# Performance work log

Hardware: AMD Instinct MI355X
Metric: run time of the kernel (lower is better)

## Reference

```python
import jax, jax.numpy as jnp
import numpy as np

WAVE_LEN = 1000.0
DIM_G = 64


def box_relational_embedding(boxes):
    # boxes: (B, N, 4) -> (B, N, N, 64) trigonometric geometry embedding
    B, N, _ = boxes.shape
    x_min, y_min, x_max, y_max = jnp.split(boxes, 4, axis=-1)  # each (B,N,1)
    cx = (x_min + x_max) * 0.5
    cy = (y_min + y_max) * 0.5
    w = (x_max - x_min) + 1.0
    h = (y_max - y_min) + 1.0
    cxT = jnp.swapaxes(cx, 1, 2)  # (B,1,N)
    cyT = jnp.swapaxes(cy, 1, 2)
    dx = jnp.log(jnp.clip(jnp.abs((cx - cxT) / w), 1e-3))  # (B,N,N)
    dy = jnp.log(jnp.clip(jnp.abs((cy - cyT) / h), 1e-3))
    dw = jnp.log(w / jnp.swapaxes(w, 1, 2))
    dh = jnp.log(h / jnp.swapaxes(h, 1, 2))
    pos = jnp.stack([dx, dy, dw, dh], axis=-1)  # (B,N,N,4)
    n_freq = DIM_G // 8  # 8 frequency bands
    dim_mat = 1.0 / (WAVE_LEN ** (jnp.arange(n_freq, dtype=pos.dtype) / n_freq))
    mul = (100.0 * pos)[..., None] * dim_mat  # (B,N,N,4,8)
    mul = mul.reshape(B, N, N, 4 * n_freq)  # (B,N,N,32)
    return jnp.concatenate([jnp.sin(mul), jnp.cos(mul)], axis=-1)  # (B,N,N,64)


def setup_inputs() -> dict:
    key = jax.random.key(0)
    ks = jax.random.split(key, 12)
    B, N, D, H = 32, 196, 1024, 8
    scale = 0.02
    inp = {
        "input_query": jax.random.normal(ks[0], (B, N, D), jnp.float32),
        "input_key": jax.random.normal(ks[1], (B, N, D), jnp.float32),
        "input_value": jax.random.normal(ks[2], (B, N, D), jnp.float32),
        "input_box": jax.random.uniform(ks[3], (B, N, 4), jnp.float32),
        "Wq": jax.random.normal(ks[4], (D, D), jnp.float32) * scale,
        "bq": jnp.zeros((D,), jnp.float32),
        "Wk": jax.random.normal(ks[5], (D, D), jnp.float32) * scale,
        "bk": jnp.zeros((D,), jnp.float32),
        "Wv": jax.random.normal(ks[6], (D, D), jnp.float32) * scale,
        "bv": jnp.zeros((D,), jnp.float32),
        "Wo": jax.random.normal(ks[7], (D, D), jnp.float32) * scale,
        "bo": jnp.zeros((D,), jnp.float32),
        "WG_w": jax.random.normal(ks[8], (H, DIM_G), jnp.float32) * scale,  # 8 stacked (64->1) linears
        "WG_b": jnp.zeros((H,), jnp.float32),
    }
    return inp


def reference(input_query, input_key, input_value, input_box,
              Wq, bq, Wk, bk, Wv, bv, Wo, bo, WG_w, WG_b):
    B, N, D = input_query.shape
    H = WG_w.shape[0]
    dk = D // H
    # relation geometry weights per head: (B,H,N,N)
    geo = box_relational_embedding(input_box)  # (B,N,N,64)
    wg = jax.nn.relu(jnp.einsum('bnmg,hg->bhnm', geo, WG_w) + WG_b[None, :, None, None])
    # projections (torch Linear: x @ W.T + b), reshape to (B,H,N,dk)
    def proj(x, W, b):
        return (x @ W.T + b).reshape(B, N, H, dk).transpose(0, 2, 1, 3)
    q = proj(input_query, Wq, bq)
    k = proj(input_key, Wk, bk)
    v = proj(input_value, Wv, bv)
    scores = jnp.einsum('bhnd,bhmd->bhnm', q, k) / np.sqrt(dk).astype(q.dtype)
    logits = jnp.log(jnp.clip(wg, 1e-6)) + scores
    attn = jax.nn.softmax(logits, axis=-1)  # (B,H,N,N)
    out = jnp.einsum('bhnm,bhmd->bhnd', attn, v)  # (B,H,N,dk)
    out = out.transpose(0, 2, 1, 3).reshape(B, N, D)
    return out @ Wo.T + bo
```

## Files before the change

### kernel.cpp

```cpp
#include <hip/hip_runtime.h>
#include <hip/hip_bf16.h>

typedef __bf16 bf16;
typedef _Float16 half_t;
typedef bf16 bf16x8 __attribute__((ext_vector_type(8)));
typedef bf16 bf16x4 __attribute__((ext_vector_type(4)));
typedef float floatx4 __attribute__((ext_vector_type(4)));

#define B_ 32
#define N_ 196
#define H_ 8
#define D_ 1024
#define DK_ 128
#define BN_ (B_ * N_)
#define BH_ (B_ * H_)
#define NPAD_ 224
#define PSTRIDE_ 232

#define KT_ 16

typedef __attribute__((address_space(3))) unsigned int lds_uint;
typedef const __attribute__((address_space(1))) unsigned int glb_uint;

__device__ __forceinline__ void async_copy16(const bf16* g, bf16* l) {
  __builtin_amdgcn_global_load_lds((glb_uint*)g, (lds_uint*)l, 16, 0, 0);
}

#define BARRIER() asm volatile("s_barrier" ::: "memory")
#define WAITV0() asm volatile("s_waitcnt vmcnt(0)" ::: "memory")

__global__ __launch_bounds__(256) void cvt3_kernel(const float* __restrict__ s0,
                                                   const float* __restrict__ s1,
                                                   const float* __restrict__ s2,
                                                   bf16* __restrict__ d0,
                                                   bf16* __restrict__ d1,
                                                   bf16* __restrict__ d2, int n4) {
  const int which = blockIdx.y;
  const float* s = (which == 0) ? s0 : (which == 1) ? s1 : s2;
  bf16* d = (which == 0) ? d0 : (which == 1) ? d1 : d2;
  int i = blockIdx.x * 256 + threadIdx.x;
  if (i >= n4) return;
  float4 v = ((const float4*)s)[i];
  bf16x4 o;
  o[0] = (bf16)v.x;
  o[1] = (bf16)v.y;
  o[2] = (bf16)v.z;
  o[3] = (bf16)v.w;
  *(bf16x4*)(d + (size_t)i * 4) = o;
}

__global__ __launch_bounds__(256) void cvt4_kernel(const float* __restrict__ s0,
                                                   const float* __restrict__ s1,
                                                   const float* __restrict__ s2,
                                                   const float* __restrict__ s3,
                                                   bf16* __restrict__ d0,
                                                   bf16* __restrict__ d1,
                                                   bf16* __restrict__ d2,
                                                   bf16* __restrict__ d3, int n4) {
  const int which = blockIdx.y;
  const float* s = (which == 0) ? s0 : (which == 1) ? s1 : (which == 2) ? s2 : s3;
  bf16* d = (which == 0) ? d0 : (which == 1) ? d1 : (which == 2) ? d2 : d3;
  int i = blockIdx.x * 256 + threadIdx.x;
  if (i >= n4) return;
  float4 v = ((const float4*)s)[i];
  bf16x4 o;
  o[0] = (bf16)v.x;
  o[1] = (bf16)v.y;
  o[2] = (bf16)v.z;
  o[3] = (bf16)v.w;
  *(bf16x4*)(d + (size_t)i * 4) = o;
}

__global__ __launch_bounds__(256) void geo_kernel(const float* __restrict__ box,
                                                  const float* __restrict__ WGw,
                                                  const float* __restrict__ WGb,
                                                  half_t* __restrict__ S) {
  __shared__ float4 wsh[128];
  if (threadIdx.x < 128) wsh[threadIdx.x] = ((const float4*)WGw)[threadIdx.x];
  __syncthreads();

  int tid = blockIdx.x * 256 + threadIdx.x;
  int b = tid / (N_ * N_);
  int rem = tid - b * (N_ * N_);
  int n = rem / N_;
  int m = rem - n * N_;

  float4 bn = ((const float4*)box)[b * N_ + n];
  float4 bm = ((const float4*)box)[b * N_ + m];
  float cxn = (bn.x + bn.z) * 0.5f, cyn = (bn.y + bn.w) * 0.5f;
  float wn = bn.z - bn.x + 1.0f, hn = bn.w - bn.y + 1.0f;
  float cxm = (bm.x + bm.z) * 0.5f, cym = (bm.y + bm.w) * 0.5f;
  float wm = bm.z - bm.x + 1.0f, hm = bm.w - bm.y + 1.0f;

  float pos[4];
  pos[0] = __logf(fmaxf(fabsf((cxn - cxm) / wn), 1e-3f));
  pos[1] = __logf(fmaxf(fabsf((cyn - cym) / hn), 1e-3f));
  pos[2] = __logf(wn / wm);
  pos[3] = __logf(hn / hm);

  const float dims[8] = {1.0f,          0.4216965034f, 0.1778279410f, 0.0749894209f,
                         0.0316227766f, 0.0133352143f, 0.0056234133f, 0.0023713737f};
  float feat[64];
#pragma unroll
  for (int p = 0; p < 4; p++) {
#pragma unroll
    for (int f = 0; f < 8; f++) {
      float a = 100.0f * pos[p] * dims[f];
      feat[p * 8 + f] = __sinf(a);
      feat[32 + p * 8 + f] = __cosf(a);
    }
  }
#pragma unroll
  for (int hh = 0; hh < 8; hh++) {
    float accv = WGb[hh];
#pragma unroll
    for (int g4 = 0; g4 < 16; g4++) {
      float4 wv = wsh[hh * 16 + g4];
      accv += feat[g4 * 4 + 0] * wv.x + feat[g4 * 4 + 1] * wv.y +
              feat[g4 * 4 + 2] * wv.z + feat[g4 * 4 + 3] * wv.w;
    }
    S[((size_t)((b * H_ + hh) * N_ + n)) * NPAD_ + m] = (half_t)fmaxf(accv, 1e-6f);
  }
}

template <int VARIANT>
__global__ __launch_bounds__(256, 2) void gemm2p(
    const bf16* __restrict__ A0, const bf16* __restrict__ A1, const bf16* __restrict__ A2,
    const bf16* __restrict__ W0, const bf16* __restrict__ W1, const bf16* __restrict__ W2,
    const float* __restrict__ b0, const float* __restrict__ b1, const float* __restrict__ b2,
    void* __restrict__ O0, void* __restrict__ O1, void* __restrict__ O2) {
  __shared__ bf16 As[2][128 * 64];
  __shared__ bf16 Bs[2][128 * 64];

  const int NZ = (VARIANT == 0) ? 3 : 1;
  const int chunk = 49 * NZ;
  const int f = blockIdx.x + (blockIdx.y << 3) + blockIdx.z * 392;
  const int L = (f & 7) * chunk + (f >> 3);
  const int lx = L & 7;
  const int lyz = L >> 3;
  const int ly = (VARIANT == 0) ? (lyz % 49) : lyz;
  const int z = (VARIANT == 0) ? (lyz / 49) : 0;

  const bf16* A = (z == 0) ? A0 : (z == 1) ? A1 : A2;
  const bf16* W = (z == 0) ? W0 : (z == 1) ? W1 : W2;
  const float* bias = (z == 0) ? b0 : (z == 1) ? b1 : b2;

  const int tid = threadIdx.x;
  const int lane = tid & 63;
  const int wid = tid >> 6;
  const int l16 = lane & 15;
  const int quad = lane >> 4;
  const int wm = wid >> 1;
  const int wn = wid & 1;

  const bf16* gA = A + (size_t)ly * 128 * D_;
  const bf16* gB = W + (size_t)lx * 128 * D_;

  const int srow = tid >> 3;
  const int lslot = (tid & 7) ^ (srow & 7);
  size_t sOff[4];
#pragma unroll
  for (int u = 0; u < 4; u++) sOff[u] = (size_t)(u * 32 + srow) * D_ + lslot * 8;

  int arow[4], brow[4], kslot[2];
#pragma unroll
  for (int i = 0; i < 4; i++) arow[i] = (wm * 64 + i * 16 + l16) * 64;
#pragma unroll
  for (int j = 0; j < 4; j++) brow[j] = (wn * 64 + j * 16 + l16) * 64;
#pragma unroll
  for (int kk = 0; kk < 2; kk++) kslot[kk] = ((kk * 4 + quad) ^ (l16 & 7)) * 8;

  floatx4 acc[4][4];
#pragma unroll
  for (int i = 0; i < 4; i++)
#pragma unroll
    for (int j = 0; j < 4; j++)
#pragma unroll
      for (int r = 0; r < 4; r++) acc[i][j][r] = 0.0f;

#pragma unroll
  for (int u = 0; u < 4; u++) {
    async_copy16(gA + sOff[u], &As[0][u * 2048 + tid * 8]);
    async_copy16(gB + sOff[u], &Bs[0][u * 2048 + tid * 8]);
  }
  WAITV0();
  BARRIER();

  for (int kt = 0; kt < KT_; ++kt) {
    const int cur = kt & 1;
    const bf16* Ab = As[cur];
    const bf16* Bb = Bs[cur];
    const bool pf = (kt + 1 < KT_);
    const bf16* pa = gA + (kt + 1) * 64;
    const bf16* pb = gB + (kt + 1) * 64;
    bf16* dA = As[cur ^ 1];
    bf16* dB = Bs[cur ^ 1];
    bf16x8 af[4], bfv[4];

#pragma unroll
    for (int i = 0; i < 4; i++) af[i] = *(const bf16x8*)(Ab + arow[i] + kslot[0]);
#pragma unroll
    for (int j = 0; j < 4; j++) bfv[j] = *(const bf16x8*)(Bb + brow[j] + kslot[0]);
    if (pf) {
#pragma unroll
      for (int u = 0; u < 4; u++) async_copy16(pa + sOff[u], dA + u * 2048 + tid * 8);
    }
    __builtin_amdgcn_s_setprio(1);
#pragma unroll
    for (int i = 0; i < 4; i++)
#pragma unroll
      for (int j = 0; j < 4; j++)
        acc[i][j] = __builtin_amdgcn_mfma_f32_16x16x32_bf16(af[i], bfv[j], acc[i][j], 0, 0, 0);
    __builtin_amdgcn_s_setprio(0);

#pragma unroll
    for (int i = 0; i < 4; i++) af[i] = *(const bf16x8*)(Ab + arow[i] + kslot[1]);
#pragma unroll
    for (int j = 0; j < 4; j++) bfv[j] = *(const bf16x8*)(Bb + brow[j] + kslot[1]);
    if (pf) {
#pragma unroll
      for (int u = 0; u < 4; u++) async_copy16(pb + sOff[u], dB + u * 2048 + tid * 8);
    }
    __builtin_amdgcn_s_setprio(1);
#pragma unroll
    for (int i = 0; i < 4; i++)
#pragma unroll
      for (int j = 0; j < 4; j++)
        acc[i][j] = __builtin_amdgcn_mfma_f32_16x16x32_bf16(af[i], bfv[j], acc[i][j], 0, 0, 0);
    __builtin_amdgcn_s_setprio(0);

    if (pf) {
      WAITV0();
      BARRIER();
    }
  }

  const int m0 = ly * 128 + wm * 64;
  const int n0 = lx * 128 + wn * 64;
#pragma unroll
  for (int j = 0; j < 4; j++) {
    const int col = n0 + j * 16 + l16;
    const float bv = bias[col];
#pragma unroll
    for (int i = 0; i < 4; i++) {
#pragma unroll
      for (int r = 0; r < 4; r++) {
        const int row = m0 + i * 16 + quad * 4 + r;
        float v = acc[i][j][r] + bv;
        if (VARIANT == 1) {
          ((float*)O0)[(size_t)row * D_ + col] = v;
        } else if (z < 2) {
          bf16* Cout = z ? (bf16*)O1 : (bf16*)O0;
          Cout[(size_t)row * D_ + col] = (bf16)v;
        } else {
          int b = row / N_;
          int n = row - b * N_;
          int h = col >> 7;
          int d = col & (DK_ - 1);
          ((bf16*)O2)[((size_t)((b * H_ + h) * DK_ + d)) * NPAD_ + n] = (bf16)v;
        }
      }
    }
  }
}

__global__ __launch_bounds__(256) void attn_kernel(const bf16* __restrict__ Q,
                                                   const bf16* __restrict__ Kmat,
                                                   const bf16* __restrict__ Vt,
                                                   const half_t* __restrict__ Sb,
                                                   bf16* __restrict__ AO) {
  __shared__ bf16 Ks[7 * 4096];
  __shared__ bf16 Vs[7 * 4096];
  __shared__ bf16 Pl[4 * 16 * PSTRIDE_];

  const int bh = blockIdx.x;
  const int b = bh >> 3;
  const int h = bh & 7;
  const int tid = threadIdx.x;
  const int wave = tid >> 6;
  const int lane = tid & 63;
  const int l16 = lane & 15;
  const int quad = lane >> 4;

  size_t kSrc[2];
  int kDst[2];
#pragma unroll
  for (int u = 0; u < 2; u++) {
    const int slot = u * 256 + tid;
    const int srow = slot >> 4;
    const int scs = slot & 15;
    kSrc[u] = (size_t)(b * N_ + srow) * D_ + h * DK_ + (scs ^ (srow & 7)) * 8;
    kDst[u] = slot * 8;
  }
  size_t vSrc[2];
#pragma unroll
  for (int u = 0; u < 2; u++) {
    const int slot = u * 256 + tid;
    const int vrow = slot >> 2;
    const int vcs = slot & 3;
    vSrc[u] = (size_t)bh * DK_ * NPAD_ + (size_t)vrow * NPAD_ + (vcs ^ (vrow & 3)) * 8;
  }

#pragma unroll
  for (int jt = 0; jt < 7; ++jt) {
    const size_t koff = (size_t)(jt * 32) * D_;
#pragma unroll
    for (int u = 0; u < 2; u++) async_copy16(Kmat + kSrc[u] + koff, Ks + jt * 4096 + kDst[u]);
  }
#pragma unroll
  for (int t7 = 0; t7 < 7; ++t7) {
#pragma unroll
    for (int u = 0; u < 2; u++) async_copy16(Vt + vSrc[u] + t7 * 32, Vs + t7 * 4096 + kDst[u]);
  }
  WAITV0();
  BARRIER();

  const float scale = 0.08838834764831845f;
  const half_t* bbase = Sb + ((size_t)bh * N_) * NPAD_;
  bf16* pw = Pl + wave * 16 * PSTRIDE_;
  const bf16* pr = pw + l16 * PSTRIDE_ + quad * 8;

  for (int rt = 0; rt < 4; ++rt) {
    const int nrb = rt * 64 + wave * 16;

    const int na = nrb + l16;
    const bool nav = na < N_;
    const bf16* aptr = Q + ((size_t)(b * N_ + (nav ? na : 0))) * D_ + h * DK_ + quad * 8;
    bf16x8 afr[4];
#pragma unroll
    for (int kk = 0; kk < 4; kk++) {
      bf16x8 v = *(const bf16x8*)(aptr + kk * 32);
      if (!nav) {
#pragma unroll
        for (int e = 0; e < 8; e++) v[e] = (bf16)0.0f;
      }
      afr[kk] = v;
    }

    floatx4 S[14];
#pragma unroll
    for (int j = 0; j < 14; j++)
#pragma unroll
      for (int r = 0; r < 4; r++) S[j][r] = 0.0f;

#pragma unroll
    for (int jt = 0; jt < 7; ++jt) {
      const bf16* Kb = Ks + jt * 4096;
      __builtin_amdgcn_s_setprio(1);
#pragma unroll
      for (int jj = 0; jj < 2; jj++) {
        const int mloc = jj * 16 + l16;
#pragma unroll
        for (int kk = 0; kk < 4; kk++) {
          bf16x8 bb = *(const bf16x8*)(Kb + mloc * 128 + ((kk * 4 + quad) ^ (l16 & 7)) * 8);
          S[jt * 2 + jj] = __builtin_amdgcn_mfma_f32_16x16x32_bf16(afr[kk], bb, S[jt * 2 + jj], 0, 0, 0);
        }
      }
      __builtin_amdgcn_s_setprio(0);
    }

    float inv[4];
#pragma unroll
    for (int r = 0; r < 4; r++) {
      const int n = nrb + quad * 4 + r;
      const bool nv = n < N_;
      const size_t brow = (size_t)(nv ? n : 0) * NPAD_;
      float mx = -1e30f;
#pragma unroll
      for (int j = 0; j < 14; j++) {
        const int m = j * 16 + l16;
        float s = (nv && m < N_) ? S[j][r] * scale : -1e30f;
        S[j][r] = s;
        mx = fmaxf(mx, s);
      }
#pragma unroll
      for (int off = 1; off < 16; off <<= 1) mx = fmaxf(mx, __shfl_xor(mx, off, 64));
      float sum = 0.0f;
#pragma unroll
      for (int j = 0; j < 14; j++) {
        const int m = j * 16 + l16;
        float w = (m < N_) ? (float)bbase[brow + m] : 0.0f;
        float e = w * __expf(S[j][r] - mx);
        sum += e;
        pw[(quad * 4 + r) * PSTRIDE_ + m] = (bf16)e;
      }
#pragma unroll
      for (int off = 1; off < 16; off <<= 1) sum += __shfl_xor(sum, off, 64);
      inv[r] = 1.0f / sum;
    }

    floatx4 O[8];
#pragma unroll
    for (int j2 = 0; j2 < 8; j2++)
#pragma unroll
      for (int r = 0; r < 4; r++) O[j2][r] = 0.0f;

#pragma unroll
    for (int t7 = 0; t7 < 7; ++t7) {
      const bf16* Vb = Vs + t7 * 4096;
      bf16x8 a = *(const bf16x8*)(pr + t7 * 32);
      __builtin_amdgcn_s_setprio(1);
#pragma unroll
      for (int j2 = 0; j2 < 8; j2++) {
        bf16x8 bb = *(const bf16x8*)(Vb + (j2 * 16 + l16) * 32 + (quad ^ (l16 & 3)) * 8);
        O[j2] = __builtin_amdgcn_mfma_f32_16x16x32_bf16(a, bb, O[j2], 0, 0, 0);
      }
      __builtin_amdgcn_s_setprio(0);
    }

#pragma unroll
    for (int r = 0; r < 4; r++) {
      const int n = nrb + quad * 4 + r;
      if (n < N_) {
#pragma unroll
        for (int j2 = 0; j2 < 8; j2++) {
          AO[((size_t)(b * N_ + n)) * D_ + h * DK_ + j2 * 16 + l16] = (bf16)(O[j2][r] * inv[r]);
        }
      }
    }
  }
}

extern "C" void kernel_launch(void* const* d_in, const int* in_sizes, int n_in,
                              void* d_out, int out_size, void* d_ws, size_t ws_size,
                              hipStream_t stream) {
  const float* xq = (const float*)d_in[0];
  const float* xk = (const float*)d_in[1];
  const float* xv = (const float*)d_in[2];
  const float* box = (const float*)d_in[3];
  const float* Wq = (const float*)d_in[4];
  const float* bq = (const float*)d_in[5];
  const float* Wk = (const float*)d_in[6];
  const float* bk = (const float*)d_in[7];
  const float* Wv = (const float*)d_in[8];
  const float* bv = (const float*)d_in[9];
  const float* Wo = (const float*)d_in[10];
  const float* bo = (const float*)d_in[11];
  const float* WGw = (const float*)d_in[12];
  const float* WGb = (const float*)d_in[13];

  size_t off = 0;
  char* wsc = (char*)d_ws;
  auto alloc = [&](size_t bytes) -> void* {
    void* p = wsc + off;
    off += (bytes + 255) & ~(size_t)255;
    return p;
  };
  bf16* xq_b = (bf16*)alloc((size_t)BN_ * D_ * 2);
  bf16* xk_b = (bf16*)alloc((size_t)BN_ * D_ * 2);
  bf16* xv_b = (bf16*)alloc((size_t)BN_ * D_ * 2);
  bf16* wq_b = (bf16*)alloc((size_t)D_ * D_ * 2);
  bf16* wk_b = (bf16*)alloc((size_t)D_ * D_ * 2);
  bf16* wv_b = (bf16*)alloc((size_t)D_ * D_ * 2);
  bf16* wo_b = (bf16*)alloc((size_t)D_ * D_ * 2);
  bf16* q_b = (bf16*)alloc((size_t)BN_ * D_ * 2);
  bf16* k_b = (bf16*)alloc((size_t)BN_ * D_ * 2);
  bf16* vt_b = (bf16*)alloc((size_t)BH_ * DK_ * NPAD_ * 2);
  bf16* ao_b = (bf16*)alloc((size_t)BN_ * D_ * 2);
  half_t* S = (half_t*)alloc((size_t)BH_ * N_ * NPAD_ * 2);

  const int n4x = BN_ * D_ / 4;
  const int n4w = D_ * D_ / 4;
  dim3 g3(n4x / 256, 3, 1);
  cvt3_kernel<<<g3, 256, 0, stream>>>(xq, xk, xv, xq_b, xk_b, xv_b, n4x);
  dim3 g4(n4w / 256, 4, 1);
  cvt4_kernel<<<g4, 256, 0, stream>>>(Wq, Wk, Wv, Wo, wq_b, wk_b, wv_b, wo_b, n4w);

  geo_kernel<<<(B_ * N_ * N_) / 256, 256, 0, stream>>>(box, WGw, WGb, S);

  hipMemsetAsync(vt_b, 0, (size_t)BH_ * DK_ * NPAD_ * 2, stream);

  dim3 gqkv(D_ / 128, BN_ / 128, 3);
  gemm2p<0><<<gqkv, 256, 0, stream>>>(xq_b, xk_b, xv_b, wq_b, wk_b, wv_b, bq, bk, bv,
                                      q_b, k_b, vt_b);

  attn_kernel<<<BH_, 256, 0, stream>>>(q_b, k_b, vt_b, S, ao_b);

  dim3 gout(D_ / 128, BN_ / 128, 1);
  gemm2p<1><<<gout, 256, 0, stream>>>(ao_b, nullptr, nullptr, wo_b, nullptr, nullptr,
                                      bo, nullptr, nullptr, d_out, nullptr, nullptr);
}
```

Before: 317.0 us.

## Switch projection GEMMs to 256x256 tiles with 8 waves and padded M

Replaces the 128x128, 4-wave GEMM with a 512-thread kernel computing 256x256 output tiles, each wave owning a 128x64 sub-tile. The M dimension is padded to 6400 rows and the stores are row-guarded. This raises arithmetic intensity per LDS load and cuts global traffic for the QKV and output projections. It also issues both prefetches at the top of each k-step and drops the custom L2-friendly block swizzle. The costs are fewer blocks (300 for QKV, 100 for the output projection) on a chip with many CUs, higher register pressure from 32 accumulators, 64KB of LDS per block, and wasted work on the padded rows.

```diff
diff --git a/kernel.cpp b/kernel.cpp
--- a/kernel.cpp
+++ b/kernel.cpp
@@ -14,6 +14,7 @@
 #define DK_ 128
 #define BN_ (B_ * N_)
 #define BH_ (B_ * H_)
+#define MPAD_ 6400
 #define NPAD_ 224
 #define PSTRIDE_ 232
 
@@ -124,23 +125,15 @@
 }
 
 template <int VARIANT>
-__global__ __launch_bounds__(256, 2) void gemm2p(
+__global__ __launch_bounds__(512) void gemm8w(
     const bf16* __restrict__ A0, const bf16* __restrict__ A1, const bf16* __restrict__ A2,
     const bf16* __restrict__ W0, const bf16* __restrict__ W1, const bf16* __restrict__ W2,
     const float* __restrict__ b0, const float* __restrict__ b1, const float* __restrict__ b2,
     void* __restrict__ O0, void* __restrict__ O1, void* __restrict__ O2) {
-  __shared__ bf16 As[2][128 * 64];
-  __shared__ bf16 Bs[2][128 * 64];
-
-  const int NZ = (VARIANT == 0) ? 3 : 1;
-  const int chunk = 49 * NZ;
-  const int f = blockIdx.x + (blockIdx.y << 3) + blockIdx.z * 392;
-  const int L = (f & 7) * chunk + (f >> 3);
-  const int lx = L & 7;
-  const int lyz = L >> 3;
-  const int ly = (VARIANT == 0) ? (lyz % 49) : lyz;
-  const int z = (VARIANT == 0) ? (lyz / 49) : 0;
-
+  __shared__ bf16 As[2][256 * 64];
+  __shared__ bf16 Bs[2][256 * 64];
+
+  const int z = (VARIANT == 0) ? blockIdx.z : 0;
   const bf16* A = (z == 0) ? A0 : (z == 1) ? A1 : A2;
   const bf16* W = (z == 0) ? W0 : (z == 1) ? W1 : W2;
   const float* bias = (z == 0) ? b0 : (z == 1) ? b1 : b2;
@@ -150,29 +143,29 @@
   const int wid = tid >> 6;
   const int l16 = lane & 15;
   const int quad = lane >> 4;
-  const int wm = wid >> 1;
-  const int wn = wid & 1;
-
-  const bf16* gA = A + (size_t)ly * 128 * D_;
-  const bf16* gB = W + (size_t)lx * 128 * D_;
+  const int wm = wid >> 2;
+  const int wn = wid & 3;
+
+  const bf16* gA = A + (size_t)blockIdx.y * 256 * D_;
+  const bf16* gB = W + (size_t)blockIdx.x * 256 * D_;
 
   const int srow = tid >> 3;
   const int lslot = (tid & 7) ^ (srow & 7);
   size_t sOff[4];
 #pragma unroll
-  for (int u = 0; u < 4; u++) sOff[u] = (size_t)(u * 32 + srow) * D_ + lslot * 8;
-
-  int arow[4], brow[4], kslot[2];
-#pragma unroll
-  for (int i = 0; i < 4; i++) arow[i] = (wm * 64 + i * 16 + l16) * 64;
+  for (int u = 0; u < 4; u++) sOff[u] = (size_t)(u * 64 + srow) * D_ + lslot * 8;
+
+  int arow[8], brow[4], kslot[2];
+#pragma unroll
+  for (int i = 0; i < 8; i++) arow[i] = (wm * 128 + i * 16 + l16) * 64;
 #pragma unroll
   for (int j = 0; j < 4; j++) brow[j] = (wn * 64 + j * 16 + l16) * 64;
 #pragma unroll
   for (int kk = 0; kk < 2; kk++) kslot[kk] = ((kk * 4 + quad) ^ (l16 & 7)) * 8;
 
-  floatx4 acc[4][4];
-#pragma unroll
-  for (int i = 0; i < 4; i++)
+  floatx4 acc[8][4];
+#pragma unroll
+  for (int i = 0; i < 8; i++)
 #pragma unroll
     for (int j = 0; j < 4; j++)
 #pragma unroll
@@ -180,54 +173,52 @@
 
 #pragma unroll
   for (int u = 0; u < 4; u++) {
-    async_copy16(gA + sOff[u], &As[0][u * 2048 + tid * 8]);
-    async_copy16(gB + sOff[u], &Bs[0][u * 2048 + tid * 8]);
+    async_copy16(gA + sOff[u], &As[0][(u * 512 + tid) * 8]);
+    async_copy16(gB + sOff[u], &Bs[0][(u * 512 + tid) * 8]);
   }
   WAITV0();
   BARRIER();
 
   for (int kt = 0; kt < KT_; ++kt) {
     const int cur = kt & 1;
+    const bool pf = (kt + 1 < KT_);
+    if (pf) {
+      const bf16* pa = gA + (kt + 1) * 64;
+      const bf16* pb = gB + (kt + 1) * 64;
+#pragma unroll
+      for (int u = 0; u < 4; u++) {
+        async_copy16(pa + sOff[u], &As[cur ^ 1][(u * 512 + tid) * 8]);
+        async_copy16(pb + sOff[u], &Bs[cur ^ 1][(u * 512 + tid) * 8]);
+      }
+    }
     const bf16* Ab = As[cur];
     const bf16* Bb = Bs[cur];
-    const bool pf = (kt + 1 < KT_);
-    const bf16* pa = gA + (kt + 1) * 64;
-    const bf16* pb = gB + (kt + 1) * 64;
-    bf16* dA = As[cur ^ 1];
-    bf16* dB = Bs[cur ^ 1];
-    bf16x8 af[4], bfv[4];
-
-#pragma unroll
-    for (int i = 0; i < 4; i++) af[i] = *(const bf16x8*)(Ab + arow[i] + kslot[0]);
-#pragma unroll
-    for (int j = 0; j < 4; j++) bfv[j] = *(const bf16x8*)(Bb + brow[j] + kslot[0]);
-    if (pf) {
-#pragma unroll
-      for (int u = 0; u < 4; u++) async_copy16(pa + sOff[u], dA + u * 2048 + tid * 8);
-    }
-    __builtin_amdgcn_s_setprio(1);
-#pragma unroll
-    for (int i = 0; i < 4; i++)
-#pragma unroll
-      for (int j = 0; j < 4; j++)
-        acc[i][j] = __builtin_amdgcn_mfma_f32_16x16x32_bf16(af[i], bfv[j], acc[i][j], 0, 0, 0);
-    __builtin_amdgcn_s_setprio(0);
-
-#pragma unroll
-    for (int i = 0; i < 4; i++) af[i] = *(const bf16x8*)(Ab + arow[i] + kslot[1]);
-#pragma unroll
-    for (int j = 0; j < 4; j++) bfv[j] = *(const bf16x8*)(Bb + brow[j] + kslot[1]);
-    if (pf) {
-#pragma unroll
-      for (int u = 0; u < 4; u++) async_copy16(pb + sOff[u], dB + u * 2048 + tid * 8);
-    }
-    __builtin_amdgcn_s_setprio(1);
-#pragma unroll
-    for (int i = 0; i < 4; i++)
-#pragma unroll
-      for (int j = 0; j < 4; j++)
-        acc[i][j] = __builtin_amdgcn_mfma_f32_16x16x32_bf16(af[i], bfv[j], acc[i][j], 0, 0, 0);
-    __builtin_amdgcn_s_setprio(0);
+
+    bf16x8 bfv[4][2];
+#pragma unroll
+    for (int j = 0; j < 4; j++)
+#pragma unroll
+      for (int kk = 0; kk < 2; kk++) bfv[j][kk] = *(const bf16x8*)(Bb + brow[j] + kslot[kk]);
+
+#pragma unroll
+    for (int p = 0; p < 4; p++) {
+      bf16x8 af[2][2];
+#pragma unroll
+      for (int i2 = 0; i2 < 2; i2++)
+#pragma unroll
+        for (int kk = 0; kk < 2; kk++)
+          af[i2][kk] = *(const bf16x8*)(Ab + arow[p * 2 + i2] + kslot[kk]);
+      __builtin_amdgcn_s_setprio(1);
+#pragma unroll
+      for (int i2 = 0; i2 < 2; i2++)
+#pragma unroll
+        for (int j = 0; j < 4; j++)
+#pragma unroll
+          for (int kk = 0; kk < 2; kk++)
+            acc[p * 2 + i2][j] = __builtin_amdgcn_mfma_f32_16x16x32_bf16(
+                af[i2][kk], bfv[j][kk], acc[p * 2 + i2][j], 0, 0, 0);
+      __builtin_amdgcn_s_setprio(0);
+    }
 
     if (pf) {
       WAITV0();
@@ -235,29 +226,31 @@
     }
   }
 
-  const int m0 = ly * 128 + wm * 64;
-  const int n0 = lx * 128 + wn * 64;
+  const int m0 = blockIdx.y * 256 + wm * 128;
+  const int n0 = blockIdx.x * 256 + wn * 64;
 #pragma unroll
   for (int j = 0; j < 4; j++) {
     const int col = n0 + j * 16 + l16;
     const float bv = bias[col];
 #pragma unroll
-    for (int i = 0; i < 4; i++) {
+    for (int i = 0; i < 8; i++) {
 #pragma unroll
       for (int r = 0; r < 4; r++) {
         const int row = m0 + i * 16 + quad * 4 + r;
-        float v = acc[i][j][r] + bv;
-        if (VARIANT == 1) {
-          ((float*)O0)[(size_t)row * D_ + col] = v;
-        } else if (z < 2) {
-          bf16* Cout = z ? (bf16*)O1 : (bf16*)O0;
-          Cout[(size_t)row * D_ + col] = (bf16)v;
-        } else {
-          int b = row / N_;
-          int n = row - b * N_;
-          int h = col >> 7;
-          int d = col & (DK_ - 1);
-          ((bf16*)O2)[((size_t)((b * H_ + h) * DK_ + d)) * NPAD_ + n] = (bf16)v;
+        if (row < BN_) {
+          float v = acc[i][j][r] + bv;
+          if (VARIANT == 1) {
+            ((float*)O0)[(size_t)row * D_ + col] = v;
+          } else if (z < 2) {
+            bf16* Cout = z ? (bf16*)O1 : (bf16*)O0;
+            Cout[(size_t)row * D_ + col] = (bf16)v;
+          } else {
+            int b = row / N_;
+            int n = row - b * N_;
+            int h = col >> 7;
+            int d = col & (DK_ - 1);
+            ((bf16*)O2)[((size_t)((b * H_ + h) * DK_ + d)) * NPAD_ + n] = (bf16)v;
+          }
         }
       }
     }
@@ -446,9 +439,9 @@
     off += (bytes + 255) & ~(size_t)255;
     return p;
   };
-  bf16* xq_b = (bf16*)alloc((size_t)BN_ * D_ * 2);
-  bf16* xk_b = (bf16*)alloc((size_t)BN_ * D_ * 2);
-  bf16* xv_b = (bf16*)alloc((size_t)BN_ * D_ * 2);
+  bf16* xq_b = (bf16*)alloc((size_t)MPAD_ * D_ * 2);
+  bf16* xk_b = (bf16*)alloc((size_t)MPAD_ * D_ * 2);
+  bf16* xv_b = (bf16*)alloc((size_t)MPAD_ * D_ * 2);
   bf16* wq_b = (bf16*)alloc((size_t)D_ * D_ * 2);
   bf16* wk_b = (bf16*)alloc((size_t)D_ * D_ * 2);
   bf16* wv_b = (bf16*)alloc((size_t)D_ * D_ * 2);
@@ -456,7 +449,7 @@
   bf16* q_b = (bf16*)alloc((size_t)BN_ * D_ * 2);
   bf16* k_b = (bf16*)alloc((size_t)BN_ * D_ * 2);
   bf16* vt_b = (bf16*)alloc((size_t)BH_ * DK_ * NPAD_ * 2);
-  bf16* ao_b = (bf16*)alloc((size_t)BN_ * D_ * 2);
+  bf16* ao_b = (bf16*)alloc((size_t)MPAD_ * D_ * 2);
   half_t* S = (half_t*)alloc((size_t)BH_ * N_ * NPAD_ * 2);
 
   const int n4x = BN_ * D_ / 4;
@@ -470,13 +463,13 @@
 
   hipMemsetAsync(vt_b, 0, (size_t)BH_ * DK_ * NPAD_ * 2, stream);
 
-  dim3 gqkv(D_ / 128, BN_ / 128, 3);
-  gemm2p<0><<<gqkv, 256, 0, stream>>>(xq_b, xk_b, xv_b, wq_b, wk_b, wv_b, bq, bk, bv,
+  dim3 gqkv(D_ / 256, MPAD_ / 256, 3);
+  gemm8w<0><<<gqkv, 512, 0, stream>>>(xq_b, xk_b, xv_b, wq_b, wk_b, wv_b, bq, bk, bv,
                                       q_b, k_b, vt_b);
 
   attn_kernel<<<BH_, 256, 0, stream>>>(q_b, k_b, vt_b, S, ao_b);
 
-  dim3 gout(D_ / 128, BN_ / 128, 1);
-  gemm2p<1><<<gout, 256, 0, stream>>>(ao_b, nullptr, nullptr, wo_b, nullptr, nullptr,
+  dim3 gout(D_ / 256, MPAD_ / 256, 1);
+  gemm8w<1><<<gout, 512, 0, stream>>>(ao_b, nullptr, nullptr, wo_b, nullptr, nullptr,
                                       bo, nullptr, nullptr, d_out, nullptr, nullptr);
 }
```

New measurement: 383.0 us. 1.21x slower.
